# Optimization experiments

Hardware: AMD Instinct MI355X
Metric: run time of the kernel (lower is better)

The kernel has to match this reference:

```python
import jax, jax.numpy as jnp
import numpy as np
from jax import lax

B, S, H, T = 64, 512, 1024, 67


def setup_inputs() -> dict:
    key = jax.random.key(0)
    ks = jax.random.split(key, 8)
    hidden = jax.random.normal(ks[0], (B, S, H), jnp.float32)
    labels = jax.random.randint(ks[1], (B, S), 0, T)
    lengths = jax.random.randint(ks[2], (B,), S // 2, S + 1)
    mask = (jnp.arange(S)[None, :] < lengths[:, None]).astype(jnp.int32)  # prefix mask, mask[:,0]=1
    W = jax.random.normal(ks[3], (H, T), jnp.float32) * 0.02
    b = jnp.zeros((T,), jnp.float32)
    start_trans = jax.random.uniform(ks[4], (T,), jnp.float32, -0.1, 0.1)
    end_trans = jax.random.uniform(ks[5], (T,), jnp.float32, -0.1, 0.1)
    trans = jax.random.uniform(ks[6], (T, T), jnp.float32, -0.1, 0.1)
    return dict(hidden=hidden, labels=labels, mask=mask, W=W, b=b,
                start_trans=start_trans, end_trans=end_trans, trans=trans)


def _crf_llh(em, tags, mask, start_trans, end_trans, trans):
    # em: (B,S,T), tags: (B,S) int, mask: (B,S) bool. torchcrf log-likelihood per sequence.
    maskf = mask.astype(em.dtype)
    # numerator: score of the gold path
    em_tag = jnp.take_along_axis(em, tags[:, :, None], axis=2)[:, :, 0]       # (B,S)
    num = start_trans[tags[:, 0]] + em_tag[:, 0]
    trans_tag = trans[tags[:, :-1], tags[:, 1:]]                              # (B,S-1)
    num = num + jnp.sum((trans_tag + em_tag[:, 1:]) * maskf[:, 1:], axis=1)
    last_idx = jnp.sum(mask.astype(jnp.int32), axis=1) - 1                    # (B,)
    last_tags = jnp.take_along_axis(tags, last_idx[:, None], axis=1)[:, 0]
    num = num + end_trans[last_tags]
    # denominator: log partition via forward algorithm (scan over time)
    def step(score, x):
        em_i, m_i = x  # (B,T), (B,)
        nxt = jax.nn.logsumexp(score[:, :, None] + trans[None] + em_i[:, None, :], axis=1)
        return jnp.where(m_i[:, None], nxt, score), None
    init = start_trans[None, :] + em[:, 0]
    score, _ = lax.scan(step, init, (em[:, 1:].transpose(1, 0, 2), mask[:, 1:].T))
    denom = jax.nn.logsumexp(score + end_trans[None, :], axis=1)
    return num - denom


def _viterbi(em, mask, start_trans, end_trans, trans):
    # returns best tag sequence (B,S), padded positions set to 0
    n_tags = em.shape[-1]
    ident = jnp.arange(n_tags)[None, :]
    def fwd(score, x):
        em_i, m_i = x  # (B,T), (B,)
        cand = score[:, :, None] + trans[None]                                # (B,T,T)
        idx = jnp.argmax(cand, axis=1)                                        # (B,T)
        nxt = jnp.max(cand, axis=1) + em_i
        score = jnp.where(m_i[:, None], nxt, score)
        idx = jnp.where(m_i[:, None], idx, ident)  # identity link on padded steps
        return score, idx
    init = start_trans[None, :] + em[:, 0]
    score, hist = lax.scan(fwd, init, (em[:, 1:].transpose(1, 0, 2), mask[:, 1:].T))
    best = jnp.argmax(score + end_trans[None, :], axis=1)                     # (B,)
    def back(carry, h):  # carry = tag at t+1, h = hist[t]: (B,T)
        prev = jnp.take_along_axis(h, carry[:, None], axis=1)[:, 0]
        return prev, prev
    _, ys = lax.scan(back, best, hist, reverse=True)                          # (S-1,B) tags[0..S-2]
    tags = jnp.concatenate([ys.transpose(1, 0), best[:, None]], axis=1)       # (B,S)
    return jnp.where(mask, tags, 0)


def reference(hidden, labels, mask, W, b, start_trans, end_trans, trans):
    maskb = mask.astype(bool)
    # dropout is identity in eval mode
    em = jnp.einsum('bsh,ht->bst', jax.nn.leaky_relu(hidden, 0.01), W) + b     # token_scores
    llh = _crf_llh(em, labels, maskb, start_trans, end_trans, trans)
    loss = -jnp.sum(llh) / em.shape[0]
    tags = _viterbi(em, maskb, start_trans, end_trans, trans)
    return loss, tags, em
```

## Files before the change

kernel.cpp:

```cpp
#include <hip/hip_runtime.h>

#define Bn 64
#define Sn 512
#define Hn 1024
#define Tn 67

#define LOG2E 1.4426950408889634f
#define LN2   0.6931471805599453f

__global__ __launch_bounds__(256) void gemm_em(
    const float* __restrict__ hidden, const float* __restrict__ W,
    const float* __restrict__ bias, float* __restrict__ em,
    float* __restrict__ out)
{
    __shared__ __align__(16) float hs[64][36];
    __shared__ __align__(16) float wt[80][36];

    const int tid = threadIdx.x;
    const int tx = tid & 15, ty = tid >> 4;
    const int row0 = blockIdx.x * 64;

    if (blockIdx.x == 0 && tid == 0) out[0] = 0.0f;

    float acc[4][5];
#pragma unroll
    for (int u = 0; u < 4; ++u)
#pragma unroll
        for (int v = 0; v < 5; ++v) acc[u][v] = 0.f;

    for (int kc = 0; kc < Hn; kc += 32) {
#pragma unroll
        for (int l = 0; l < 2; ++l) {
            int idx = tid + l * 256;
            int r = idx >> 3, kq = (idx & 7) << 2;
            float4 v = *reinterpret_cast<const float4*>(
                &hidden[(size_t)(row0 + r) * Hn + kc + kq]);
            v.x = v.x > 0.f ? v.x : 0.01f * v.x;
            v.y = v.y > 0.f ? v.y : 0.01f * v.y;
            v.z = v.z > 0.f ? v.z : 0.01f * v.z;
            v.w = v.w > 0.f ? v.w : 0.01f * v.w;
            *reinterpret_cast<float4*>(&hs[r][kq]) = v;
        }
        for (int idx = tid; idx < 32 * Tn; idx += 256) {
            int k = idx / Tn;
            int t = idx - k * Tn;
            wt[t][k] = W[(size_t)(kc + k) * Tn + t];
        }
        __syncthreads();

#pragma unroll
        for (int k0 = 0; k0 < 32; k0 += 4) {
            float4 hv[4], wv[5];
#pragma unroll
            for (int u = 0; u < 4; ++u)
                hv[u] = *reinterpret_cast<float4*>(&hs[ty + 16 * u][k0]);
#pragma unroll
            for (int v = 0; v < 5; ++v)
                wv[v] = *reinterpret_cast<float4*>(&wt[tx + 16 * v][k0]);
#pragma unroll
            for (int u = 0; u < 4; ++u)
#pragma unroll
                for (int v = 0; v < 5; ++v) {
                    acc[u][v] = fmaf(hv[u].x, wv[v].x, acc[u][v]);
                    acc[u][v] = fmaf(hv[u].y, wv[v].y, acc[u][v]);
                    acc[u][v] = fmaf(hv[u].z, wv[v].z, acc[u][v]);
                    acc[u][v] = fmaf(hv[u].w, wv[v].w, acc[u][v]);
                }
        }
        __syncthreads();
    }

#pragma unroll
    for (int v = 0; v < 5; ++v) {
        int c = tx + 16 * v;
        if (c < Tn) {
            float bb = bias[c];
#pragma unroll
            for (int u = 0; u < 4; ++u) {
                int row = row0 + ty + 16 * u;
                em[(size_t)row * Tn + c] = acc[u][v] + bb;
            }
        }
    }
}

__global__ __launch_bounds__(256) void crf_scan2(
    const float* __restrict__ em, const int* __restrict__ labels,
    const int* __restrict__ mask, const float* __restrict__ startT,
    const float* __restrict__ endT, const float* __restrict__ trans,
    float* __restrict__ out)
{
    __shared__ __align__(16) float pbuf[2][72];
    __shared__ __align__(16) float vbuf[2][72];
    __shared__ __align__(16) float em_lds[2][32 * Tn];
    __shared__ int mask_lds[Sn];
    __shared__ unsigned char hist[Sn - 1][68];
    __shared__ int tg[Sn];
    __shared__ float redf[256];
    __shared__ int redi[256];

    const int tid = threadIdx.x;
    const int wid = tid >> 6;
    const int lane = tid & 63;
    const int b = blockIdx.x;
    const bool isCRF = wid < 2;
    const bool hiw = (wid & 1);
    const int st = hiw ? (64 + (lane < 3 ? lane : 2)) : lane;
    const bool active = (!hiw) || (lane < 3);
    const float* emg = em + (size_t)b * Sn * Tn;

    for (int i = tid; i < 32 * Tn; i += 256) em_lds[0][i] = emg[i];
    for (int i = tid; i < Sn; i += 256) mask_lds[i] = mask[b * Sn + i];
    if (tid == 0) {
        pbuf[0][67] = 0.f; pbuf[1][67] = 0.f;
        vbuf[0][67] = -1e30f; vbuf[1][67] = -1e30f;
    }
    __syncthreads();

    float sc = startT[st] + em_lds[0][st];
    if (isCRF) { if (active) pbuf[1][st] = sc; }
    else       { if (active) vbuf[0][st] = sc; }
    __syncthreads();
    if (isCRF) {
        float M0 = pbuf[1][0];
        float p = exp2f((sc - M0) * LOG2E);
        if (active) pbuf[0][st] = p;
        if (tid == 0) { pbuf[0][68] = sc; pbuf[0][69] = M0; }
    }
    __syncthreads();

    int bufc = 0;
    if (isCRF) {
        float Ecol[68];
#pragma unroll
        for (int i = 0; i < Tn; ++i) Ecol[i] = exp2f(trans[i * Tn + st] * LOG2E);
        Ecol[67] = 0.f;

        for (int t = 1; t < Sn; ++t) {
            if ((t & 31) == 1) {
                int k = (t >> 5) + 1;
                if (k < 16) {
                    const float* src = emg + (size_t)k * 32 * Tn;
                    float* dst = em_lds[k & 1];
                    for (int i = tid; i < 32 * Tn; i += 128) dst[i] = src[i];
                }
            }
            const float* row = em_lds[(t >> 5) & 1] + (t & 31) * Tn;
            float em_t = row[st];
            int m = mask_lds[t];
            float M_used = pbuf[bufc][69];
            float sc0p   = pbuf[bufc][68];
            const float4* P = (const float4*)&pbuf[bufc][0];
            float a0 = 0.f, a1 = 0.f, a2 = 0.f, a3 = 0.f;
#pragma unroll
            for (int q = 0; q < 17; ++q) {
                float4 pv = P[q];
                a0 = fmaf(pv.x, Ecol[4 * q + 0], a0);
                a1 = fmaf(pv.y, Ecol[4 * q + 1], a1);
                a2 = fmaf(pv.z, Ecol[4 * q + 2], a2);
                a3 = fmaf(pv.w, Ecol[4 * q + 3], a3);
            }
            float aa = (a0 + a1) + (a2 + a3);
            float nxt = M_used + log2f(aa) * LN2 + em_t;
            if (m) sc = nxt;
            float Mn = sc0p;
            float p = exp2f((sc - Mn) * LOG2E);
            int nb = bufc ^ 1;
            if (active) pbuf[nb][st] = p;
            if (tid == 0) { pbuf[nb][68] = sc; pbuf[nb][69] = Mn; }
            __syncthreads();
            bufc = nb;
        }
    } else {
        float Tcol[68];
#pragma unroll
        for (int i = 0; i < Tn; ++i) Tcol[i] = trans[i * Tn + st];
        Tcol[67] = 0.f;

        for (int t = 1; t < Sn; ++t) {
            const float* row = em_lds[(t >> 5) & 1] + (t & 31) * Tn;
            float em_t = row[st];
            int m = mask_lds[t];
            const float4* Vp = (const float4*)&vbuf[bufc][0];
            float bvv[34]; int bx[34];
#pragma unroll
            for (int q = 0; q < 17; ++q) {
                float4 v = Vp[q];
                float c0 = v.x + Tcol[4 * q + 0];
                float c1 = v.y + Tcol[4 * q + 1];
                float c2 = v.z + Tcol[4 * q + 2];
                float c3 = v.w + Tcol[4 * q + 3];
                bool r0 = c1 > c0;
                bvv[2 * q]     = r0 ? c1 : c0;
                bx[2 * q]      = r0 ? 4 * q + 1 : 4 * q + 0;
                bool r1 = c3 > c2;
                bvv[2 * q + 1] = r1 ? c3 : c2;
                bx[2 * q + 1]  = r1 ? 4 * q + 3 : 4 * q + 2;
            }
#pragma unroll
            for (int q = 0; q < 17; ++q) {
                bool r = bvv[2 * q + 1] > bvv[2 * q];
                bvv[q] = r ? bvv[2 * q + 1] : bvv[2 * q];
                bx[q]  = r ? bx[2 * q + 1]  : bx[2 * q];
            }
#pragma unroll
            for (int q = 0; q < 8; ++q) {
                bool r = bvv[2 * q + 1] > bvv[2 * q];
                bvv[q] = r ? bvv[2 * q + 1] : bvv[2 * q];
                bx[q]  = r ? bx[2 * q + 1]  : bx[2 * q];
            }
            bvv[8] = bvv[16]; bx[8] = bx[16];
#pragma unroll
            for (int q = 0; q < 4; ++q) {
                bool r = bvv[2 * q + 1] > bvv[2 * q];
                bvv[q] = r ? bvv[2 * q + 1] : bvv[2 * q];
                bx[q]  = r ? bx[2 * q + 1]  : bx[2 * q];
            }
            bvv[4] = bvv[8]; bx[4] = bx[8];
#pragma unroll
            for (int q = 0; q < 2; ++q) {
                bool r = bvv[2 * q + 1] > bvv[2 * q];
                bvv[q] = r ? bvv[2 * q + 1] : bvv[2 * q];
                bx[q]  = r ? bx[2 * q + 1]  : bx[2 * q];
            }
            bvv[2] = bvv[4]; bx[2] = bx[4];
            { bool r = bvv[1] > bvv[0]; bvv[0] = r ? bvv[1] : bvv[0]; bx[0] = r ? bx[1] : bx[0]; }
            { bool r = bvv[2] > bvv[0]; bvv[0] = r ? bvv[2] : bvv[0]; bx[0] = r ? bx[2] : bx[0]; }

            float nv = bvv[0] + em_t;
            int idx = m ? bx[0] : st;
            if (m) sc = nv;
            int nb = bufc ^ 1;
            if (active) {
                hist[t - 1][st] = (unsigned char)idx;
                vbuf[nb][st] = sc;
            }
            __syncthreads();
            bufc = nb;
        }
    }

    if (isCRF) { if (active) pbuf[0][st] = sc + endT[st]; }
    else       { if (active) vbuf[0][st] = sc + endT[st]; }
    __syncthreads();

    float part = 0.f; int lenp = 0;
    for (int s = tid; s < Sn; s += 256) {
        int ms = mask_lds[s];
        lenp += ms;
        int ls = labels[b * Sn + s];
        if (s == 0) {
            part += startT[ls] + emg[ls];
        } else if (ms) {
            int lp = labels[b * Sn + s - 1];
            part += trans[lp * Tn + ls] + emg[(size_t)s * Tn + ls];
        }
    }
    redf[tid] = part; redi[tid] = lenp;
    __syncthreads();

    if (tid == 0) {
        float mx = -1e30f;
        for (int i = 0; i < Tn; ++i) mx = fmaxf(mx, pbuf[0][i]);
        float ss = 0.f;
        for (int i = 0; i < Tn; ++i) ss += exp2f((pbuf[0][i] - mx) * LOG2E);
        float denom = mx + log2f(ss) * LN2;
        float num = 0.f; int len = 0;
        for (int i = 0; i < 256; ++i) { num += redf[i]; len += redi[i]; }
        int last = labels[b * Sn + len - 1];
        num += endT[last];
        atomicAdd(out, -(num - denom) * (1.0f / (float)Bn));
    }
    if (tid == 128) {
        float best = -1e30f; int bi = 0;
        for (int i = 0; i < Tn; ++i) {
            float c = vbuf[0][i];
            if (c > best) { best = c; bi = i; }
        }
        int carry = bi;
        tg[Sn - 1] = carry;
        for (int k = Sn - 2; k >= 0; --k) {
            carry = hist[k][carry];
            tg[k] = carry;
        }
    }
    __syncthreads();

    float* tagsOut = out + 1 + b * Sn;
    for (int s = tid; s < Sn; s += 256)
        tagsOut[s] = mask_lds[s] ? (float)tg[s] : 0.f;
}

extern "C" void kernel_launch(void* const* d_in, const int* in_sizes, int n_in,
                              void* d_out, int out_size, void* d_ws, size_t ws_size,
                              hipStream_t stream) {
    const float* hidden = (const float*)d_in[0];
    const int*   labels = (const int*)d_in[1];
    const int*   maskp  = (const int*)d_in[2];
    const float* W      = (const float*)d_in[3];
    const float* bias   = (const float*)d_in[4];
    const float* startT = (const float*)d_in[5];
    const float* endT   = (const float*)d_in[6];
    const float* trans  = (const float*)d_in[7];
    float* out = (float*)d_out;
    float* em  = out + 1 + (size_t)Bn * Sn;

    hipLaunchKernelGGL(gemm_em, dim3((Bn * Sn) / 64), dim3(256), 0, stream,
                       hidden, W, bias, em, out);
    hipLaunchKernelGGL(crf_scan2, dim3(Bn), dim3(256), 0, stream,
                       em, labels, maskp, startT, endT, trans, out);
}
```

Baseline: 712.7 us.

## Restructure CRF scan into single-wave forward and Viterbi loops without block barriers

The CRF kernel drops from 256 to 192 threads with one role per wave. Wave 0 runs the whole forward logsumexp recursion, each lane covering one tag plus, for three lanes, a second tag. Wave 1 runs Viterbi, with the three extra tags resolved by packed 64-bit argmax keys reduced through cross-lane shuffles. Wave 2 computes the gold-path numerator, and emissions are prefetched through registers into padded LDS tiles. This removes the block-wide __syncthreads on every time step, at the cost of more per-lane work and shuffle traffic on the serial critical path.

New measurement: 789.6 us. 1.11x slower.

```diff
diff --git a/kernel.cpp b/kernel.cpp
--- a/kernel.cpp
+++ b/kernel.cpp
@@ -84,112 +84,216 @@
     }
 }
 
-__global__ __launch_bounds__(256) void crf_scan2(
+__device__ __forceinline__ unsigned long long shflx64(unsigned long long v, int m) {
+    unsigned int lo = (unsigned int)v, hi = (unsigned int)(v >> 32);
+    lo = __shfl_xor(lo, m);
+    hi = __shfl_xor(hi, m);
+    return ((unsigned long long)hi << 32) | lo;
+}
+
+__device__ __forceinline__ unsigned long long packkey(float v, int idx) {
+    unsigned int b = __float_as_uint(v);
+    unsigned int s = b ^ (unsigned int)(((int)b >> 31) | 0x80000000);
+    return ((unsigned long long)s << 32) | (unsigned int)(127 - idx);
+}
+
+__device__ __forceinline__ float unpackval(unsigned long long key) {
+    unsigned int s = (unsigned int)(key >> 32);
+    unsigned int b = s ^ (unsigned int)((~(int)s >> 31) | 0x80000000);
+    return __uint_as_float(b);
+}
+
+__global__ __launch_bounds__(192) void crf_scan3(
     const float* __restrict__ em, const int* __restrict__ labels,
     const int* __restrict__ mask, const float* __restrict__ startT,
     const float* __restrict__ endT, const float* __restrict__ trans,
     float* __restrict__ out)
 {
-    __shared__ __align__(16) float pbuf[2][72];
-    __shared__ __align__(16) float vbuf[2][72];
-    __shared__ __align__(16) float em_lds[2][32 * Tn];
-    __shared__ int mask_lds[Sn];
+    __shared__ __align__(16) float emC[2][1088];
+    __shared__ __align__(16) float emV[2][1088];
+    __shared__ int maskC[Sn];
+    __shared__ int maskV[Sn];
+    __shared__ __align__(16) float pb[2][72];
+    __shared__ __align__(16) float vb[2][72];
     __shared__ unsigned char hist[Sn - 1][68];
     __shared__ int tg[Sn];
-    __shared__ float redf[256];
-    __shared__ int redi[256];
+    __shared__ float numSh;
+    __shared__ int lenSh;
 
     const int tid = threadIdx.x;
     const int wid = tid >> 6;
     const int lane = tid & 63;
     const int b = blockIdx.x;
-    const bool isCRF = wid < 2;
-    const bool hiw = (wid & 1);
-    const int st = hiw ? (64 + (lane < 3 ? lane : 2)) : lane;
-    const bool active = (!hiw) || (lane < 3);
     const float* emg = em + (size_t)b * Sn * Tn;
-
-    for (int i = tid; i < 32 * Tn; i += 256) em_lds[0][i] = emg[i];
-    for (int i = tid; i < Sn; i += 256) mask_lds[i] = mask[b * Sn + i];
-    if (tid == 0) {
-        pbuf[0][67] = 0.f; pbuf[1][67] = 0.f;
-        vbuf[0][67] = -1e30f; vbuf[1][67] = -1e30f;
-    }
-    __syncthreads();
-
-    float sc = startT[st] + em_lds[0][st];
-    if (isCRF) { if (active) pbuf[1][st] = sc; }
-    else       { if (active) vbuf[0][st] = sc; }
-    __syncthreads();
-    if (isCRF) {
-        float M0 = pbuf[1][0];
-        float p = exp2f((sc - M0) * LOG2E);
-        if (active) pbuf[0][st] = p;
-        if (tid == 0) { pbuf[0][68] = sc; pbuf[0][69] = M0; }
-    }
-    __syncthreads();
-
-    int bufc = 0;
-    if (isCRF) {
-        float Ecol[68];
-#pragma unroll
-        for (int i = 0; i < Tn; ++i) Ecol[i] = exp2f(trans[i * Tn + st] * LOG2E);
-        Ecol[67] = 0.f;
+    const int u2 = lane < 3 ? lane : 2;
+    const int st2 = 64 + u2;
+
+    if (wid == 0) {
+#pragma unroll
+        for (int i = 0; i < 8; ++i)
+            maskC[lane + i * 64] = mask[b * Sn + lane + i * 64];
+
+        float Ec1[68], Ec2[68];
+#pragma unroll
+        for (int i = 0; i < Tn; ++i) {
+            Ec1[i] = exp2f(trans[i * Tn + lane] * LOG2E);
+            Ec2[i] = exp2f(trans[i * Tn + st2] * LOG2E);
+        }
+        Ec1[67] = 0.f; Ec2[67] = 0.f;
+
+        float sreg[17];
+#pragma unroll
+        for (int i = 0; i < 17; ++i) { int idx = lane + i * 64; if (idx > 1071) idx = 1071; sreg[i] = emg[idx]; }
+#pragma unroll
+        for (int i = 0; i < 17; ++i) {
+            int idx = lane + i * 64;
+            if (idx < 1072) { int s = idx / 67; emC[0][s * 68 + (idx - s * 67)] = sreg[i]; }
+        }
+#pragma unroll
+        for (int i = 0; i < 17; ++i) { int idx = lane + i * 64; if (idx > 1071) idx = 1071; sreg[i] = emg[1072 + idx]; }
+
+        if (lane == 0) { pb[0][67] = 0.f; pb[1][67] = 0.f; }
+
+        float sc1 = startT[lane] + emC[0][lane];
+        float sc2 = startT[st2] + emC[0][st2];
+        float M = __shfl(sc1, 0);
+        float p1 = exp2f((sc1 - M) * LOG2E);
+        float p2 = exp2f((sc2 - M) * LOG2E);
+        pb[0][lane] = p1;
+        if (lane < 3) pb[0][64 + lane] = p2;
+        float Mprev = M;
 
         for (int t = 1; t < Sn; ++t) {
-            if ((t & 31) == 1) {
-                int k = (t >> 5) + 1;
-                if (k < 16) {
-                    const float* src = emg + (size_t)k * 32 * Tn;
-                    float* dst = em_lds[k & 1];
-                    for (int i = tid; i < 32 * Tn; i += 128) dst[i] = src[i];
+            const int cb = (t >> 4) & 1;
+            if ((t & 15) == 0) {
+                const int k = t >> 4;
+#pragma unroll
+                for (int i = 0; i < 17; ++i) {
+                    int idx = lane + i * 64;
+                    if (idx < 1072) { int s = idx / 67; emC[cb][s * 68 + (idx - s * 67)] = sreg[i]; }
                 }
-            }
-            const float* row = em_lds[(t >> 5) & 1] + (t & 31) * Tn;
-            float em_t = row[st];
-            int m = mask_lds[t];
-            float M_used = pbuf[bufc][69];
-            float sc0p   = pbuf[bufc][68];
-            const float4* P = (const float4*)&pbuf[bufc][0];
-            float a0 = 0.f, a1 = 0.f, a2 = 0.f, a3 = 0.f;
+                if (k < 31) {
+                    const float* src = emg + (size_t)(k + 1) * 1072;
+#pragma unroll
+                    for (int i = 0; i < 17; ++i) { int idx = lane + i * 64; if (idx > 1071) idx = 1071; sreg[i] = src[idx]; }
+                }
+            }
+            const float* row = &emC[cb][(t & 15) * 68];
+            float em1 = row[lane];
+            float em2 = row[st2];
+            int m = maskC[t];
+            const float4* P = (const float4*)&pb[(t + 1) & 1][0];
+            float a0 = 0, a1 = 0, a2 = 0, a3 = 0, c0 = 0, c1 = 0, c2 = 0, c3 = 0;
 #pragma unroll
             for (int q = 0; q < 17; ++q) {
                 float4 pv = P[q];
-                a0 = fmaf(pv.x, Ecol[4 * q + 0], a0);
-                a1 = fmaf(pv.y, Ecol[4 * q + 1], a1);
-                a2 = fmaf(pv.z, Ecol[4 * q + 2], a2);
-                a3 = fmaf(pv.w, Ecol[4 * q + 3], a3);
-            }
-            float aa = (a0 + a1) + (a2 + a3);
-            float nxt = M_used + log2f(aa) * LN2 + em_t;
-            if (m) sc = nxt;
-            float Mn = sc0p;
-            float p = exp2f((sc - Mn) * LOG2E);
-            int nb = bufc ^ 1;
-            if (active) pbuf[nb][st] = p;
-            if (tid == 0) { pbuf[nb][68] = sc; pbuf[nb][69] = Mn; }
-            __syncthreads();
-            bufc = nb;
-        }
-    } else {
-        float Tcol[68];
-#pragma unroll
-        for (int i = 0; i < Tn; ++i) Tcol[i] = trans[i * Tn + st];
-        Tcol[67] = 0.f;
+                a0 = fmaf(pv.x, Ec1[4 * q + 0], a0); c0 = fmaf(pv.x, Ec2[4 * q + 0], c0);
+                a1 = fmaf(pv.y, Ec1[4 * q + 1], a1); c1 = fmaf(pv.y, Ec2[4 * q + 1], c1);
+                a2 = fmaf(pv.z, Ec1[4 * q + 2], a2); c2 = fmaf(pv.z, Ec2[4 * q + 2], c2);
+                a3 = fmaf(pv.w, Ec1[4 * q + 3], a3); c3 = fmaf(pv.w, Ec2[4 * q + 3], c3);
+            }
+            float s1 = (a0 + a1) + (a2 + a3);
+            float s2 = (c0 + c1) + (c2 + c3);
+            float n1 = Mprev + log2f(s1) * LN2 + em1;
+            float n2 = Mprev + log2f(s2) * LN2 + em2;
+            if (m) { sc1 = n1; sc2 = n2; }
+            M = __shfl(sc1, 0);
+            p1 = exp2f((sc1 - M) * LOG2E);
+            p2 = exp2f((sc2 - M) * LOG2E);
+            float* Wp = &pb[t & 1][0];
+            Wp[lane] = p1;
+            if (lane < 3) Wp[64 + lane] = p2;
+            Mprev = M;
+        }
+
+        float* F = &pb[0][0];
+        F[lane] = sc1 + endT[lane];
+        if (lane < 3) F[64 + lane] = sc2 + endT[64 + lane];
+        if (lane == 0) F[67] = -1e30f;
+        float mx = -1e30f;
+        const float4* Fv = (const float4*)F;
+#pragma unroll
+        for (int q = 0; q < 17; ++q) {
+            float4 v = Fv[q];
+            mx = fmaxf(mx, fmaxf(fmaxf(v.x, v.y), fmaxf(v.z, v.w)));
+        }
+        float ss = 0.f;
+#pragma unroll
+        for (int q = 0; q < 17; ++q) {
+            float4 v = Fv[q];
+            ss += exp2f((v.x - mx) * LOG2E) + exp2f((v.y - mx) * LOG2E)
+                + exp2f((v.z - mx) * LOG2E) + exp2f((v.w - mx) * LOG2E);
+        }
+        float denom = mx + log2f(ss) * LN2;
+        __syncthreads();
+        if (lane == 0) {
+            int len = lenSh;
+            float num = numSh + endT[labels[b * Sn + len - 1]];
+            atomicAdd(out, -(num - denom) * (1.0f / (float)Bn));
+        }
+    } else if (wid == 1) {
+#pragma unroll
+        for (int i = 0; i < 8; ++i)
+            maskV[lane + i * 64] = mask[b * Sn + lane + i * 64];
+
+        float Tc1[68];
+#pragma unroll
+        for (int i = 0; i < Tn; ++i) Tc1[i] = trans[i * Tn + lane];
+        Tc1[67] = 0.f;
+        float Tsf[3], Tss[3];
+        const int rsec = (lane < 3) ? (64 + lane) : 0;
+#pragma unroll
+        for (int u = 0; u < 3; ++u) {
+            Tsf[u] = trans[lane * Tn + 64 + u];
+            Tss[u] = trans[rsec * Tn + 64 + u];
+        }
+
+        float sreg[17];
+#pragma unroll
+        for (int i = 0; i < 17; ++i) { int idx = lane + i * 64; if (idx > 1071) idx = 1071; sreg[i] = emg[idx]; }
+#pragma unroll
+        for (int i = 0; i < 17; ++i) {
+            int idx = lane + i * 64;
+            if (idx < 1072) { int s = idx / 67; emV[0][s * 68 + (idx - s * 67)] = sreg[i]; }
+        }
+#pragma unroll
+        for (int i = 0; i < 17; ++i) { int idx = lane + i * 64; if (idx > 1071) idx = 1071; sreg[i] = emg[1072 + idx]; }
+
+        float sc1 = startT[lane] + emV[0][lane];
+        float sc2 = startT[st2] + emV[0][st2];
+        vb[0][lane] = sc1;
+        if (lane < 3) vb[0][64 + lane] = sc2;
+        if (lane == 0) { vb[0][67] = -1e30f; vb[1][67] = -1e30f; }
 
         for (int t = 1; t < Sn; ++t) {
-            const float* row = em_lds[(t >> 5) & 1] + (t & 31) * Tn;
-            float em_t = row[st];
-            int m = mask_lds[t];
-            const float4* Vp = (const float4*)&vbuf[bufc][0];
+            const int cb = (t >> 4) & 1;
+            if ((t & 15) == 0) {
+                const int k = t >> 4;
+#pragma unroll
+                for (int i = 0; i < 17; ++i) {
+                    int idx = lane + i * 64;
+                    if (idx < 1072) { int s = idx / 67; emV[cb][s * 68 + (idx - s * 67)] = sreg[i]; }
+                }
+                if (k < 31) {
+                    const float* src = emg + (size_t)(k + 1) * 1072;
+#pragma unroll
+                    for (int i = 0; i < 17; ++i) { int idx = lane + i * 64; if (idx > 1071) idx = 1071; sreg[i] = src[idx]; }
+                }
+            }
+            const float* row = &emV[cb][(t & 15) * 68];
+            float em1 = row[lane];
+            float e64 = row[64], e65 = row[65], e66 = row[66];
+            int m = maskV[t];
+
+            const float4* Vp = (const float4*)&vb[(t + 1) & 1][0];
             float bvv[34]; int bx[34];
 #pragma unroll
             for (int q = 0; q < 17; ++q) {
                 float4 v = Vp[q];
-                float c0 = v.x + Tcol[4 * q + 0];
-                float c1 = v.y + Tcol[4 * q + 1];
-                float c2 = v.z + Tcol[4 * q + 2];
-                float c3 = v.w + Tcol[4 * q + 3];
+                float c0 = v.x + Tc1[4 * q + 0];
+                float c1 = v.y + Tc1[4 * q + 1];
+                float c2 = v.z + Tc1[4 * q + 2];
+                float c3 = v.w + Tc1[4 * q + 3];
                 bool r0 = c1 > c0;
                 bvv[2 * q]     = r0 ? c1 : c0;
                 bx[2 * q]      = r0 ? 4 * q + 1 : 4 * q + 0;
@@ -226,69 +330,132 @@
             bvv[2] = bvv[4]; bx[2] = bx[4];
             { bool r = bvv[1] > bvv[0]; bvv[0] = r ? bvv[1] : bvv[0]; bx[0] = r ? bx[1] : bx[0]; }
             { bool r = bvv[2] > bvv[0]; bvv[0] = r ? bvv[2] : bvv[0]; bx[0] = r ? bx[2] : bx[0]; }
-
-            float nv = bvv[0] + em_t;
-            int idx = m ? bx[0] : st;
-            if (m) sc = nv;
-            int nb = bufc ^ 1;
-            if (active) {
-                hist[t - 1][st] = (unsigned char)idx;
-                vbuf[nb][st] = sc;
-            }
-            __syncthreads();
-            bufc = nb;
-        }
+            float n1 = bvv[0] + em1;
+
+            float ca = sc1 + Tsf[0]; int ia = lane;
+            float cbv = sc1 + Tsf[1]; int ib = lane;
+            float cc = sc1 + Tsf[2]; int ic = lane;
+            if (lane < 3) {
+                float sa = sc2 + Tss[0]; if (sa > ca)  { ca = sa;  ia = 64 + lane; }
+                float sb = sc2 + Tss[1]; if (sb > cbv) { cbv = sb; ib = 64 + lane; }
+                float scv = sc2 + Tss[2]; if (scv > cc) { cc = scv; ic = 64 + lane; }
+            }
+            unsigned long long k0 = packkey(ca, ia);
+            unsigned long long k1 = packkey(cbv, ib);
+            unsigned long long k2 = packkey(cc, ic);
+#pragma unroll
+            for (int k = 1; k < 64; k <<= 1) {
+                unsigned long long o0 = shflx64(k0, k); if (o0 > k0) k0 = o0;
+                unsigned long long o1 = shflx64(k1, k); if (o1 > k1) k1 = o1;
+                unsigned long long o2 = shflx64(k2, k); if (o2 > k2) k2 = o2;
+            }
+            float v64 = unpackval(k0) + e64;
+            float v65 = unpackval(k1) + e65;
+            float v66 = unpackval(k2) + e66;
+            int i64 = 127 - (int)(unsigned int)(k0 & 0xffffffffu);
+            int i65 = 127 - (int)(unsigned int)(k1 & 0xffffffffu);
+            int i66 = 127 - (int)(unsigned int)(k2 & 0xffffffffu);
+
+            float nuv = (lane == 0) ? v64 : (lane == 1) ? v65 : v66;
+            int nui = (lane == 0) ? i64 : (lane == 1) ? i65 : i66;
+
+            int idx1 = m ? bx[0] : lane;
+            int idx2 = m ? nui : st2;
+            if (m) { sc1 = n1; sc2 = nuv; }
+
+            hist[t - 1][lane] = (unsigned char)idx1;
+            float* Wv = &vb[t & 1][0];
+            Wv[lane] = sc1;
+            if (lane < 3) {
+                hist[t - 1][64 + lane] = (unsigned char)idx2;
+                Wv[64 + lane] = sc2;
+            }
+        }
+
+        float* F = &vb[0][0];
+        F[lane] = sc1 + endT[lane];
+        if (lane < 3) F[64 + lane] = sc2 + endT[64 + lane];
+        if (lane == 0) F[67] = -1e30f;
+        const float4* Fv = (const float4*)F;
+        float bvv[34]; int bx[34];
+#pragma unroll
+        for (int q = 0; q < 17; ++q) {
+            float4 v = Fv[q];
+            bool r0 = v.y > v.x;
+            bvv[2 * q]     = r0 ? v.y : v.x;
+            bx[2 * q]      = r0 ? 4 * q + 1 : 4 * q + 0;
+            bool r1 = v.w > v.z;
+            bvv[2 * q + 1] = r1 ? v.w : v.z;
+            bx[2 * q + 1]  = r1 ? 4 * q + 3 : 4 * q + 2;
+        }
+#pragma unroll
+        for (int q = 0; q < 17; ++q) {
+            bool r = bvv[2 * q + 1] > bvv[2 * q];
+            bvv[q] = r ? bvv[2 * q + 1] : bvv[2 * q];
+            bx[q]  = r ? bx[2 * q + 1]  : bx[2 * q];
+        }
+#pragma unroll
+        for (int q = 0; q < 8; ++q) {
+            bool r = bvv[2 * q + 1] > bvv[2 * q];
+            bvv[q] = r ? bvv[2 * q + 1] : bvv[2 * q];
+            bx[q]  = r ? bx[2 * q + 1]  : bx[2 * q];
+        }
+        bvv[8] = bvv[16]; bx[8] = bx[16];
+#pragma unroll
+        for (int q = 0; q < 4; ++q) {
+            bool r = bvv[2 * q + 1] > bvv[2 * q];
+            bvv[q] = r ? bvv[2 * q + 1] : bvv[2 * q];
+            bx[q]  = r ? bx[2 * q + 1]  : bx[2 * q];
+        }
+        bvv[4] = bvv[8]; bx[4] = bx[8];
+#pragma unroll
+        for (int q = 0; q < 2; ++q) {
+            bool r = bvv[2 * q + 1] > bvv[2 * q];
+            bvv[q] = r ? bvv[2 * q + 1] : bvv[2 * q];
+            bx[q]  = r ? bx[2 * q + 1]  : bx[2 * q];
+        }
+        bvv[2] = bvv[4]; bx[2] = bx[4];
+        { bool r = bvv[1] > bvv[0]; bvv[0] = r ? bvv[1] : bvv[0]; bx[0] = r ? bx[1] : bx[0]; }
+        { bool r = bvv[2] > bvv[0]; bvv[0] = r ? bvv[2] : bvv[0]; bx[0] = r ? bx[2] : bx[0]; }
+
+        if (lane == 0) {
+            int carry = bx[0];
+            tg[Sn - 1] = carry;
+            for (int k = Sn - 2; k >= 0; --k) {
+                carry = hist[k][carry];
+                tg[k] = carry;
+            }
+        }
+        float* tagsOut = out + 1 + b * Sn;
+#pragma unroll
+        for (int i = 0; i < 8; ++i) {
+            int s = lane + i * 64;
+            tagsOut[s] = maskV[s] ? (float)tg[s] : 0.f;
+        }
+        __syncthreads();
+    } else {
+        float part = 0.f; int lenp = 0;
+#pragma unroll
+        for (int i = 0; i < 8; ++i) {
+            int s = lane + i * 64;
+            int ms = mask[b * Sn + s];
+            lenp += ms;
+            int ls = labels[b * Sn + s];
+            if (s == 0) {
+                part += startT[ls] + emg[ls];
+            } else if (ms) {
+                int lp = labels[b * Sn + s - 1];
+                part += trans[lp * Tn + ls] + emg[(size_t)s * Tn + ls];
+            }
+        }
+#pragma unroll
+        for (int k = 1; k < 64; k <<= 1) {
+            part += __shfl_xor(part, k);
+            lenp += __shfl_xor(lenp, k);
+        }
+        if (lane == 0) { numSh = part; lenSh = lenp; }
+        __syncthreads();
     }
-
-    if (isCRF) { if (active) pbuf[0][st] = sc + endT[st]; }
-    else       { if (active) vbuf[0][st] = sc + endT[st]; }
-    __syncthreads();
-
-    float part = 0.f; int lenp = 0;
-    for (int s = tid; s < Sn; s += 256) {
-        int ms = mask_lds[s];
-        lenp += ms;
-        int ls = labels[b * Sn + s];
-        if (s == 0) {
-            part += startT[ls] + emg[ls];
-        } else if (ms) {
-            int lp = labels[b * Sn + s - 1];
-            part += trans[lp * Tn + ls] + emg[(size_t)s * Tn + ls];
-        }
-    }
-    redf[tid] = part; redi[tid] = lenp;
-    __syncthreads();
-
-    if (tid == 0) {
-        float mx = -1e30f;
-        for (int i = 0; i < Tn; ++i) mx = fmaxf(mx, pbuf[0][i]);
-        float ss = 0.f;
-        for (int i = 0; i < Tn; ++i) ss += exp2f((pbuf[0][i] - mx) * LOG2E);
-        float denom = mx + log2f(ss) * LN2;
-        float num = 0.f; int len = 0;
-        for (int i = 0; i < 256; ++i) { num += redf[i]; len += redi[i]; }
-        int last = labels[b * Sn + len - 1];
-        num += endT[last];
-        atomicAdd(out, -(num - denom) * (1.0f / (float)Bn));
-    }
-    if (tid == 128) {
-        float best = -1e30f; int bi = 0;
-        for (int i = 0; i < Tn; ++i) {
-            float c = vbuf[0][i];
-            if (c > best) { best = c; bi = i; }
-        }
-        int carry = bi;
-        tg[Sn - 1] = carry;
-        for (int k = Sn - 2; k >= 0; --k) {
-            carry = hist[k][carry];
-            tg[k] = carry;
-        }
-    }
-    __syncthreads();
-
-    float* tagsOut = out + 1 + b * Sn;
-    for (int s = tid; s < Sn; s += 256)
-        tagsOut[s] = mask_lds[s] ? (float)tg[s] : 0.f;
 }
 
 extern "C" void kernel_launch(void* const* d_in, const int* in_sizes, int n_in,
@@ -307,6 +474,6 @@
 
     hipLaunchKernelGGL(gemm_em, dim3((Bn * Sn) / 64), dim3(256), 0, stream,
                        hidden, W, bias, em, out);
-    hipLaunchKernelGGL(crf_scan2, dim3(Bn), dim3(256), 0, stream,
+    hipLaunchKernelGGL(crf_scan3, dim3(Bn), dim3(192), 0, stream,
                        em, labels, maskp, startT, endT, trans, out);
 }
```
